# Kernel optimization log

Measured on AMD Instinct MI355X. Metric: run time of the kernel, lower is better.

The kernel has to match this reference:

```python
import jax, jax.numpy as jnp
from jax import lax
import numpy as np

V, E, NF = 50000, 300, 1          # vocab, embed_size, n_features
H = 256                            # hidden size (both layers)
B, TH, TB = 128, 32, 512           # batch, headline len, body len
NC = 4                             # n_classes


def setup_inputs() -> dict:
    key = jax.random.key(0)
    ks = jax.random.split(key, 24)
    emb = jax.random.normal(ks[0], (V, E), jnp.float32) * 0.1
    emb = emb.at[0].set(0.0)  # pad token -> zero row so seqlen masking is meaningful

    def make_ids(kid, klen, T):
        raw = jax.random.randint(kid, (B, T, NF), 1, V)
        lens = jax.random.randint(klen, (B,), max(T // 4, 1), T + 1)
        mask = jnp.arange(T)[None, :, None] < lens[:, None, None]
        return jnp.where(mask, raw, 0)

    headline_ids = make_ids(ks[1], ks[2], TH)
    body_ids = make_ids(ks[3], ks[4], TB)

    def gru_params(k, din, h):
        k1, k2 = jax.random.split(k, 2)
        s = 1.0 / np.sqrt(din + h)
        return (jax.random.normal(k1, (din + h, 2 * h), jnp.float32) * s,
                jnp.ones((2 * h,), jnp.float32),          # TF GRUCell gate bias init = 1.0
                jax.random.normal(k2, (din + h, h), jnp.float32) * s,
                jnp.zeros((h,), jnp.float32))

    D0 = NF * E
    hd0 = gru_params(ks[5], D0, H)
    hd1 = gru_params(ks[6], H, H)
    bd0 = gru_params(ks[7], D0, H)
    bd1 = gru_params(ks[8], H, H)

    W_pred = jax.random.normal(ks[9], (2 * H, NC), jnp.float32) * (1.0 / np.sqrt(2 * H))
    b_pred = jnp.zeros((NC,), jnp.float32)

    out = {"headline_ids": headline_ids, "body_ids": body_ids, "embeddings": emb,
           "W_pred": W_pred, "b_pred": b_pred}
    for pref, p in (("hd0", hd0), ("hd1", hd1), ("bd0", bd0), ("bd1", bd1)):
        out[pref + "_Wg"], out[pref + "_bg"], out[pref + "_Wc"], out[pref + "_bc"] = p
    return out


def _seq_length(x):
    # used = sign(max(|x|, axis=2)); seqlen = sum over time
    return jnp.sum(jnp.sign(jnp.max(jnp.abs(x), axis=2)), axis=1).astype(jnp.int32)


def _gru_layer(x, seqlen, Wg, bg, Wc, bc):
    # x: [B, T, D] -> outputs [B, T, H], final state [B, H]; dynamic_rnn semantics:
    # past seqlen, output is zero and state is copied through.
    Bsz, T, _ = x.shape
    Hh = Wc.shape[1]
    xt = jnp.swapaxes(x, 0, 1)  # [T, B, D]
    tids = jnp.arange(T)

    def step(h, inp):
        xi, t = inp
        xh = jnp.concatenate([xi, h], axis=-1)
        r, u = jnp.split(jax.nn.sigmoid(xh @ Wg + bg), 2, axis=-1)
        c = jnp.tanh(jnp.concatenate([xi, r * h], axis=-1) @ Wc + bc)
        nh = u * h + (1.0 - u) * c
        valid = (t < seqlen)[:, None]
        out = jnp.where(valid, nh, 0.0)
        h_next = jnp.where(valid, nh, h)
        return h_next, out

    h0 = jnp.zeros((Bsz, Hh), x.dtype)
    hf, outs = lax.scan(step, h0, (xt, tids))
    return jnp.swapaxes(outs, 0, 1), hf


def _stream(ids, emb, layers):
    x = emb[ids].reshape(ids.shape[0], ids.shape[1], -1)  # [B, T, NF*E]
    h = None
    for (Wg, bg, Wc, bc) in layers:
        sl = _seq_length(x)  # recomputed from current layer inputs, as in the source
        x, h = _gru_layer(x, sl, Wg, bg, Wc, bc)
    return h


def reference(headline_ids, body_ids, embeddings,
              hd0_Wg, hd0_bg, hd0_Wc, hd0_bc, hd1_Wg, hd1_bg, hd1_Wc, hd1_bc,
              bd0_Wg, bd0_bg, bd0_Wc, bd0_bc, bd1_Wg, bd1_bg, bd1_Wc, bd1_bc,
              W_pred, b_pred):
    h_head = _stream(headline_ids, embeddings,
                     [(hd0_Wg, hd0_bg, hd0_Wc, hd0_bc), (hd1_Wg, hd1_bg, hd1_Wc, hd1_bc)])
    h_body = _stream(body_ids, embeddings,
                     [(bd0_Wg, bd0_bg, bd0_Wc, bd0_bc), (bd1_Wg, bd1_bg, bd1_Wc, bd1_bc)])
    pred_input = jnp.concatenate([h_head, h_body], axis=1)  # [B, 2H]
    return pred_input @ W_pred + b_pred                      # [B, NC]
```

## Files before the change

kernel.cpp:

```cpp
#include <hip/hip_runtime.h>
#include <cstdint>
#include <cstddef>

#define H_    256
#define NG    768
#define BATCH 128
#define TH_   32
#define TB_   512
#define E_    300
#define RPB   16
#define NBLK  (BATCH / RPB)

typedef _Float16 half8 __attribute__((ext_vector_type(8)));
typedef float    floatx4 __attribute__((ext_vector_type(4)));

#define AS1 __attribute__((address_space(1)))
#define AS3 __attribute__((address_space(3)))

#define WC_LGKM0 0xC07F
#define WC_VM14  0x0F7E
#define WC_VM6   0x0F76
#define WC_VM0   0x0F70

__global__ __launch_bounds__(256) void pack_bias(
    const float* __restrict__ bg, const float* __restrict__ bc,
    float* __restrict__ bias)
{
  int idx = blockIdx.x * 256 + threadIdx.x;
  if (idx < NG) bias[idx] = (idx < 2 * H_) ? bg[idx] : bc[idx - 2 * H_];
}

__global__ __launch_bounds__(256) void pack_bx(
    const float* __restrict__ Wg, const float* __restrict__ Wc,
    int din, int KT, _Float16* __restrict__ out)
{
  int idx = blockIdx.x * 256 + threadIdx.x;
  if (idx >= KT * 48 * 64) return;
  int lane = idx & 63, tile = idx >> 6;
  int kt = tile / 48, nt = tile - kt * 48;
  int col = nt * 16 + (lane & 15);
  int k0 = kt * 32 + (lane >> 4) * 8;
  const float* W; int ncols, c2;
  if (col < 2 * H_) { W = Wg; ncols = 2 * H_; c2 = col; }
  else              { W = Wc; ncols = H_;     c2 = col - 2 * H_; }
  _Float16* dst = out + ((size_t)(kt * 48 + nt) * 64 + lane) * 8;
#pragma unroll
  for (int j = 0; j < 8; ++j) {
    int k = k0 + j;
    dst[j] = (k < din) ? (_Float16)W[(size_t)k * ncols + c2] : (_Float16)0.f;
  }
}

__global__ __launch_bounds__(256) void pack_w(
    const float* __restrict__ Wg, const float* __restrict__ Wc, int din,
    _Float16* __restrict__ wpk)
{
  int idx = blockIdx.x * 256 + threadIdx.x;
  if (idx >= 48 * 64) return;
  int tile = idx >> 6, lane = idx & 63;
  int grp = tile >> 4, tt = tile & 15;
  int wv = tt >> 1, s = tt & 1;
  const float* W; int ncols, n0;
  if (grp == 0)      { W = Wg; ncols = 2 * H_; n0 = wv * 32 + s * 16; }
  else if (grp == 1) { W = Wg; ncols = 2 * H_; n0 = 256 + wv * 32 + s * 16; }
  else               { W = Wc; ncols = H_;     n0 = wv * 32 + s * 16; }
  int n = n0 + (lane & 15);
  int kb = (lane >> 4) * 8;
#pragma unroll
  for (int kt = 0; kt < 8; ++kt) {
    _Float16* dst = wpk + ((size_t)(tile * 8 + kt) * 64 + lane) * 8;
#pragma unroll
    for (int j = 0; j < 8; ++j)
      dst[j] = (_Float16)W[(size_t)(din + kt * 32 + kb + j) * ncols + n];
  }
}

__global__ __launch_bounds__(256) void seq_k(const int* __restrict__ ids, int T,
                                             int* __restrict__ seq)
{
  __shared__ int red[256];
  int b = blockIdx.x, tid = threadIdx.x;
  int cnt = 0;
  for (int t = tid; t < T; t += 256) cnt += (ids[b * T + t] != 0) ? 1 : 0;
  red[tid] = cnt;
  __syncthreads();
  for (int s = 128; s > 0; s >>= 1) {
    if (tid < s) red[tid] += red[tid + s];
    __syncthreads();
  }
  if (tid == 0) seq[b] = red[0];
}

__global__ __launch_bounds__(256) void gemm_mfma(
    const float* __restrict__ Adir, const int* __restrict__ ids,
    const float* __restrict__ emb,
    const _Float16* __restrict__ Bpk, const float* __restrict__ bias,
    float* __restrict__ G, int K, int KT, int t0, int tcsh, int T)
{
  __shared__ __align__(16) _Float16 Al[2][64 * 40];
  __shared__ __align__(16) _Float16 Bl[2][8 * 512];
  const int tid = threadIdx.x;
  const int w = tid >> 6, lane = tid & 63;
  const int quad = lane >> 4, l15 = lane & 15;
  const int m0 = blockIdx.x * 64;
  const int n0 = blockIdx.y * 128;
  const int tc = 1 << tcsh;

  const int am = tid >> 2, akq = tid & 3;
  const int arow = m0 + am;
  const float* asrc;
  if (Adir) {
    asrc = Adir + (size_t)arow * K;
  } else {
    int b = arow >> tcsh, tl = arow & (tc - 1);
    asrc = emb + (size_t)ids[b * T + t0 + tl] * K;
  }

  float a8[8];
  auto loadA = [&](int kt) {
    int k0 = kt * 32 + akq * 8;
#pragma unroll
    for (int j = 0; j < 8; ++j) a8[j] = (k0 + j < K) ? asrc[k0 + j] : 0.f;
  };
  auto writeA = [&](int buf) {
    half8 v;
#pragma unroll
    for (int j = 0; j < 8; ++j) v[j] = (_Float16)a8[j];
    *(half8*)&Al[buf][am * 40 + akq * 8] = v;
  };
  auto stageB = [&](int kt, int buf) {
#pragma unroll
    for (int i = 0; i < 2; ++i) {
      int nt = (n0 >> 4) + w * 2 + i;
      const _Float16* src = Bpk + ((size_t)(kt * 48 + nt) * 64 + lane) * 8;
      __builtin_amdgcn_global_load_lds(
          (const AS1 unsigned int*)src,
          (AS3 unsigned int*)&Bl[buf][(w * 2 + i) * 512 + lane * 8], 16, 0, 0);
    }
  };

  loadA(0);
  stageB(0, 0);
  writeA(0);
  floatx4 acc[4][2] = {};

  for (int kt = 0; kt < KT; ++kt) {
    const int buf = kt & 1;
    __syncthreads();
    if (kt + 1 < KT) { loadA(kt + 1); stageB(kt + 1, buf ^ 1); }
    half8 bf0 = *(const half8*)&Bl[buf][(w * 2 + 0) * 512 + lane * 8];
    half8 bf1 = *(const half8*)&Bl[buf][(w * 2 + 1) * 512 + lane * 8];
#pragma unroll
    for (int st = 0; st < 4; ++st) {
      half8 af = *(const half8*)&Al[buf][(st * 16 + l15) * 40 + quad * 8];
      acc[st][0] = __builtin_amdgcn_mfma_f32_16x16x32_f16(af, bf0, acc[st][0], 0, 0, 0);
      acc[st][1] = __builtin_amdgcn_mfma_f32_16x16x32_f16(af, bf1, acc[st][1], 0, 0, 0);
    }
    if (kt + 1 < KT) writeA(buf ^ 1);
  }

  float bb[2] = { bias[n0 + w * 32 + l15], bias[n0 + w * 32 + 16 + l15] };
#pragma unroll
  for (int s = 0; s < 2; ++s) {
    int col = n0 + w * 32 + s * 16 + l15;
    int g = col >> 8, kk = col & 255;
    int ww = kk >> 5, ss = (kk >> 4) & 1, ll = kk & 15;
    int cc = 2 * g + ss;
#pragma unroll
    for (int st = 0; st < 4; ++st) {
#pragma unroll
      for (int r = 0; r < 4; ++r) {
        int grow = m0 + st * 16 + quad * 4 + r;
        int b = grow >> tcsh, tl = grow & (tc - 1);
        int rg = b >> 4, mm = b & 15, qb = mm >> 2, rb = mm & 3;
        G[((size_t)tl * BATCH + rg * RPB) * NG +
          ((ww * 6 + cc) * 64 + qb * 16 + ll) * 4 + rb] = acc[st][s][r] + bb[s];
      }
    }
  }
}

__global__ __launch_bounds__(512, 1) void gru_pers(
    const float* __restrict__ G0, const _Float16* __restrict__ W0,
    const int* __restrict__ q0, float* __restrict__ o0, float* __restrict__ s0,
    int t00, int tc0,
    const float* __restrict__ G1, const _Float16* __restrict__ W1,
    const int* __restrict__ q1, float* __restrict__ o1, float* __restrict__ s1,
    int t01, int tc1,
    const float* __restrict__ G2, const _Float16* __restrict__ W2,
    const int* __restrict__ q2, float* __restrict__ o2, float* __restrict__ s2,
    int t02, int tc2,
    const int* __restrict__ g_ids, const float* __restrict__ g_emb,
    const _Float16* __restrict__ g_Bpk, const float* __restrict__ g_bias,
    float* __restrict__ g_G, int g_KT, int g_t0, int g_tcsh, int g_T, int g_nbx)
{
  __shared__ __align__(16) char smem[114688];

  const int tid = threadIdx.x;

  if (blockIdx.x >= 3 * NBLK) {
    const int half = tid >> 8;
    _Float16* Al = (_Float16*)(smem + half * 10240);
    _Float16* Bl = (_Float16*)(smem + 20480 + half * 16384);
    const int t256 = tid & 255;
    const int w4 = (tid >> 6) & 3, lane = tid & 63;
    const int quad = lane >> 4, l15 = lane & 15;
    const int tidx = (blockIdx.x - 3 * NBLK) * 2 + half;
    const int bx = tidx % g_nbx, by = tidx / g_nbx;
    const int m0 = bx * 64, n0 = by * 128;
    const int tc = 1 << g_tcsh;

    const int am = t256 >> 2, akq = t256 & 3;
    const int arow = m0 + am;
    const int ab = arow >> g_tcsh, atl = arow & (tc - 1);
    const float* asrc = g_emb + (size_t)g_ids[ab * g_T + g_t0 + atl] * E_;

    float a8[8];
    auto loadA = [&](int kt) {
      int k0 = kt * 32 + akq * 8;
#pragma unroll
      for (int j = 0; j < 8; ++j) a8[j] = (k0 + j < E_) ? asrc[k0 + j] : 0.f;
    };
    auto writeA = [&](int buf) {
      half8 v;
#pragma unroll
      for (int j = 0; j < 8; ++j) v[j] = (_Float16)a8[j];
      *(half8*)&Al[buf * 2560 + am * 40 + akq * 8] = v;
    };
    auto stageB = [&](int kt, int buf) {
#pragma unroll
      for (int i = 0; i < 2; ++i) {
        int nt = (n0 >> 4) + w4 * 2 + i;
        const _Float16* src = g_Bpk + ((size_t)(kt * 48 + nt) * 64 + lane) * 8;
        __builtin_amdgcn_global_load_lds(
            (const AS1 unsigned int*)src,
            (AS3 unsigned int*)&Bl[buf * 4096 + (w4 * 2 + i) * 512 + lane * 8],
            16, 0, 0);
      }
    };

    loadA(0);
    stageB(0, 0);
    writeA(0);
    floatx4 acc[4][2] = {};

    for (int kt = 0; kt < g_KT; ++kt) {
      const int buf = kt & 1;
      __syncthreads();
      if (kt + 1 < g_KT) { loadA(kt + 1); stageB(kt + 1, buf ^ 1); }
      half8 bf0 = *(const half8*)&Bl[buf * 4096 + (w4 * 2 + 0) * 512 + lane * 8];
      half8 bf1 = *(const half8*)&Bl[buf * 4096 + (w4 * 2 + 1) * 512 + lane * 8];
#pragma unroll
      for (int st = 0; st < 4; ++st) {
        half8 af = *(const half8*)&Al[buf * 2560 + (st * 16 + l15) * 40 + quad * 8];
        acc[st][0] = __builtin_amdgcn_mfma_f32_16x16x32_f16(af, bf0, acc[st][0], 0, 0, 0);
        acc[st][1] = __builtin_amdgcn_mfma_f32_16x16x32_f16(af, bf1, acc[st][1], 0, 0, 0);
      }
      if (kt + 1 < g_KT) writeA(buf ^ 1);
    }

    float bb[2] = { g_bias[n0 + w4 * 32 + l15], g_bias[n0 + w4 * 32 + 16 + l15] };
#pragma unroll
    for (int s = 0; s < 2; ++s) {
      int col = n0 + w4 * 32 + s * 16 + l15;
      int g = col >> 8, kk = col & 255;
      int ww = kk >> 5, ss = (kk >> 4) & 1, ll = kk & 15;
      int cc = 2 * g + ss;
#pragma unroll
      for (int st = 0; st < 4; ++st) {
#pragma unroll
        for (int r = 0; r < 4; ++r) {
          int grow = m0 + st * 16 + quad * 4 + r;
          int b = grow >> g_tcsh, tl = grow & (tc - 1);
          int rg2 = b >> 4, mm = b & 15, qb = mm >> 2, rb = mm & 3;
          g_G[((size_t)tl * BATCH + rg2 * RPB) * NG +
              ((ww * 6 + cc) * 64 + qb * 16 + ll) * 4 + rb] = acc[st][s][r] + bb[s];
        }
      }
    }
    return;
  }

  _Float16* hpk = (_Float16*)smem;
  _Float16* rpk = (_Float16*)(smem + 8192);
  float* GsB = (float*)(smem + 16384);

  const int job = blockIdx.x >> 3, rg = blockIdx.x & 7;
  const float* G; const _Float16* Wsrc; const int* seq;
  float* outp; float* state; int t0, tcl;
  if (job == 0)      { G = G0; Wsrc = W0; seq = q0; outp = o0; state = s0; t0 = t00; tcl = tc0; }
  else if (job == 1) { G = G1; Wsrc = W1; seq = q1; outp = o1; state = s1; t0 = t01; tcl = tc1; }
  else               { G = G2; Wsrc = W2; seq = q2; outp = o2; state = s2; t0 = t02; tcl = tc2; }
  if (!G) return;

  const int w = tid >> 6, lane = tid & 63;
  const int quad = lane >> 4, l15 = lane & 15;

  floatx4 wg[4][8];
  floatx4 wc[2][8];
#pragma unroll
  for (int i = 0; i < 4; ++i) {
    const int tile = (i >> 1) * 16 + w * 2 + (i & 1);
#pragma unroll
    for (int kt = 0; kt < 8; ++kt) {
      wg[i][kt] = *(const floatx4*)&Wsrc[((size_t)(tile * 8 + kt) * 64 + lane) * 8];
      asm volatile("" : "+v"(wg[i][kt]));
    }
  }
#pragma unroll
  for (int i = 0; i < 2; ++i) {
    const int tile = 32 + w * 2 + i;
#pragma unroll
    for (int kt = 0; kt < 8; ++kt) {
      wc[i][kt] = *(const floatx4*)&Wsrc[((size_t)(tile * 8 + kt) * 64 + lane) * 8];
      asm volatile("" : "+a"(wc[i][kt]));
    }
  }

  int seq4[4];
#pragma unroll
  for (int r = 0; r < 4; ++r) seq4[r] = seq[rg * RPB + quad * 4 + r];
  int Smax = 0;
#pragma unroll
  for (int i = 0; i < 16; ++i) Smax = max(Smax, seq[rg * RPB + i]);
  int steps = Smax - t0;
  if (steps < 0) steps = 0;
  if (steps > tcl) steps = tcl;

  const int wbase = (w * 64 + quad * 2 + (l15 >> 3)) * 8 + (l15 & 7);
  const int rbase = (((quad >> 1) << 5) + ((l15 & 3) << 3) +
                     ((l15 >> 2) << 1) + (quad & 1)) * 8;

  float h_reg[2][4];
#pragma unroll
  for (int s = 0; s < 2; ++s)
#pragma unroll
    for (int r = 0; r < 4; ++r) {
      int row = quad * 4 + r, k = w * 32 + s * 16 + l15;
      float v = (t0 == 0) ? 0.f : state[(size_t)(rg * RPB + row) * H_ + k];
      h_reg[s][r] = v;
      hpk[wbase + s * 256 + r * 64] = (_Float16)v;
    }

  const float* gblk = G + (size_t)rg * RPB * NG + w * (6 * 256);
  float* ldsw = GsB + w * (6 * 256);
  auto stage = [&](int t, int buf) {
    const float* gp = gblk + (size_t)t * BATCH * NG;
    float* lp = ldsw + buf * 12288;
#pragma unroll
    for (int c = 0; c < 6; ++c) {
      __builtin_amdgcn_global_load_lds(
          (const AS1 unsigned int*)(gp + c * 256 + lane * 4),
          (AS3 unsigned int*)(lp + c * 256), 16, 0, 0);
    }
  };
  if (steps > 0) stage(0, 0);
  __syncthreads();

  const _Float16* hA = &hpk[rbase];
  const _Float16* rA = &rpk[rbase];

  for (int t = 0; t < steps; ++t) {
    const int buf = t & 1;
    const bool staged = (t + 1 < steps);
    if (staged) stage(t + 1, buf ^ 1);

    floatx4 acc[4] = {};
#pragma unroll
    for (int kt = 0; kt < 8; ++kt) {
      half8 a = *(const half8*)&hA[kt * 512];
#pragma unroll
      for (int s = 0; s < 4; ++s)
        acc[s] = __builtin_amdgcn_mfma_f32_16x16x32_f16(
            a, __builtin_bit_cast(half8, wg[s][kt]), acc[s], 0, 0, 0);
    }

    if (staged) {
      if (outp) __builtin_amdgcn_s_waitcnt(WC_VM14);
      else      __builtin_amdgcn_s_waitcnt(WC_VM6);
    } else {
      __builtin_amdgcn_s_waitcnt(WC_VM0);
    }

    floatx4 gA[4];
#pragma unroll
    for (int c = 0; c < 4; ++c)
      gA[c] = *(const floatx4*)&GsB[buf * 12288 + (w * 6 + c) * 256 + lane * 4];

#pragma unroll
    for (int s = 0; s < 2; ++s)
#pragma unroll
      for (int r = 0; r < 4; ++r) {
        float pre = acc[s][r] + gA[s][r];
        float g = __builtin_amdgcn_rcpf(1.f + __expf(-pre));
        rpk[wbase + s * 256 + r * 64] = (_Float16)(g * h_reg[s][r]);
      }
    float u_reg[2][4];
#pragma unroll
    for (int s = 0; s < 2; ++s)
#pragma unroll
      for (int r = 0; r < 4; ++r) {
        float pre = acc[2 + s][r] + gA[2 + s][r];
        u_reg[s][r] = __builtin_amdgcn_rcpf(1.f + __expf(-pre));
      }
    __builtin_amdgcn_s_waitcnt(WC_LGKM0);
    __builtin_amdgcn_s_barrier();

    floatx4 accB[2] = {};
#pragma unroll
    for (int kt = 0; kt < 8; ++kt) {
      half8 a = *(const half8*)&rA[kt * 512];
#pragma unroll
      for (int s = 0; s < 2; ++s)
        accB[s] = __builtin_amdgcn_mfma_f32_16x16x32_f16(
            a, __builtin_bit_cast(half8, wc[s][kt]), accB[s], 0, 0, 0);
    }
    floatx4 gB[2];
#pragma unroll
    for (int s = 0; s < 2; ++s)
      gB[s] = *(const floatx4*)&GsB[buf * 12288 + (w * 6 + 4 + s) * 256 + lane * 4];

#pragma unroll
    for (int s = 0; s < 2; ++s)
#pragma unroll
      for (int r = 0; r < 4; ++r) {
        int row = quad * 4 + r;
        float pre = accB[s][r] + gB[s][r];
        float c = 1.f - 2.f * __builtin_amdgcn_rcpf(1.f + __expf(2.f * pre));
        float u = u_reg[s][r];
        float hn = u * h_reg[s][r] + (1.f - u) * c;
        bool valid = (t0 + t) < seq4[r];
        hn = valid ? hn : h_reg[s][r];
        h_reg[s][r] = hn;
        hpk[wbase + s * 256 + r * 64] = (_Float16)hn;
        if (outp)
          outp[((size_t)(rg * RPB + row) * tcl + t) * H_ + (w * 32 + s * 16 + l15)] =
              valid ? hn : 0.f;
      }
    __builtin_amdgcn_s_waitcnt(WC_LGKM0);
    __builtin_amdgcn_s_barrier();
  }
#pragma unroll
  for (int s = 0; s < 2; ++s)
#pragma unroll
    for (int r = 0; r < 4; ++r)
      state[(size_t)(rg * RPB + quad * 4 + r) * H_ + (w * 32 + s * 16 + l15)] =
          h_reg[s][r];
}

__global__ __launch_bounds__(512) void pred_k(
    const float* __restrict__ hh, const float* __restrict__ hb,
    const float* __restrict__ Wp, const float* __restrict__ bpred,
    float* __restrict__ out)
{
  int tid = threadIdx.x;
  int b = tid >> 2, c = tid & 3;
  float acc = bpred[c];
  for (int k = 0; k < H_; ++k) acc += hh[b * H_ + k] * Wp[k * 4 + c];
  for (int k = 0; k < H_; ++k) acc += hb[b * H_ + k] * Wp[(H_ + k) * 4 + c];
  out[b * 4 + c] = acc;
}

extern "C" void kernel_launch(void* const* d_in, const int* in_sizes, int n_in,
                              void* d_out, int out_size, void* d_ws, size_t ws_size,
                              hipStream_t stream)
{
  (void)in_sizes; (void)n_in; (void)out_size;
  const int*   idsH = (const int*)  d_in[0];
  const int*   idsB = (const int*)  d_in[1];
  const float* emb  = (const float*)d_in[2];
  const float* Wp   = (const float*)d_in[3];
  const float* bp   = (const float*)d_in[4];
  const float* W[4][4];
  for (int s = 0; s < 4; ++s)
    for (int q = 0; q < 4; ++q)
      W[s][q] = (const float*)d_in[5 + s * 4 + q];

  auto rnd = [](size_t n) { return (n + 255) & ~(size_t)255; };
  auto need = [&](int ch, bool rider) -> size_t {
    size_t s = 0;
    s += rnd(BATCH) * 2;
    for (int i = 0; i < 4; ++i)
      s += rnd(NG) + rnd(98304) + rnd(122880);
    s += rnd((size_t)BATCH * H_) * 4;
    s += rnd((size_t)BATCH * ch * NG) * (rider ? 2 : 1);
    s += rnd((size_t)BATCH * ch * NG);
    s += rnd((size_t)BATCH * ch * H_);
    s += rnd((size_t)BATCH * TH_ * NG);
    s += rnd((size_t)BATCH * TH_ * H_);
    return s * 4;
  };

  int CH = 64;
  bool rider = need(64, true) <= ws_size;
  bool merged = rider || need(64, false) <= ws_size;
  if (!merged) {
    while (CH > 8 && need(CH, false) > ws_size) CH >>= 1;
    merged = (CH >= TH_);
  }
  const int CHH = (CH < TH_) ? CH : TH_;
  const int tcshB = __builtin_ctz(CH), tcshH = __builtin_ctz(CHH);

  float* wbase = (float*)d_ws;
  size_t off = 0;
  auto alloc = [&](size_t n) {
    float* p = wbase + off; off += rnd(n); return p;
  };
  int* seqH = (int*)alloc(BATCH);
  int* seqB = (int*)alloc(BATCH);
  float* bi[4]; _Float16* Wpk[4]; _Float16* Bxh[4];
  const int din[4] = {E_, H_, E_, H_};
  const int KT[4]  = {10, 8, 10, 8};
  for (int s = 0; s < 4; ++s) {
    bi[s]  = alloc(NG);
    Wpk[s] = (_Float16*)alloc(98304);
    Bxh[s] = (_Float16*)alloc(122880);
  }
  float* st0  = alloc((size_t)BATCH * H_);
  float* stH0 = alloc((size_t)BATCH * H_);
  float* hfH  = alloc((size_t)BATCH * H_);
  float* hfB  = alloc((size_t)BATCH * H_);
  float* Gc0b[2];
  Gc0b[0] = alloc((size_t)BATCH * CH * NG);
  Gc0b[1] = rider ? alloc((size_t)BATCH * CH * NG) : Gc0b[0];
  float* Gc1 = alloc((size_t)BATCH * CH * NG);
  float* Oc  = alloc((size_t)BATCH * CH * H_);
  float* GH1 = alloc((size_t)BATCH * TH_ * NG);
  float* OcH = alloc((size_t)BATCH * TH_ * H_);
  float* GH0 = Gc1;

  for (int s = 0; s < 4; ++s) {
    pack_bias<<<(NG + 255) / 256, 256, 0, stream>>>(W[s][1], W[s][3], bi[s]);
    pack_w<<<(48 * 64 + 255) / 256, 256, 0, stream>>>(
        W[s][0], W[s][2], din[s], Wpk[s]);
    pack_bx<<<(KT[s] * 48 * 64 + 255) / 256, 256, 0, stream>>>(
        W[s][0], W[s][2], din[s], KT[s], Bxh[s]);
  }
  seq_k<<<BATCH, 256, 0, stream>>>(idsH, TH_, seqH);
  seq_k<<<BATCH, 256, 0, stream>>>(idsB, TB_, seqB);

  const int nbx = BATCH * CH / 64;
  const int nrider = nbx * (NG / 128) / 2;

  auto gru3 = [&](const float* g0, const _Float16* w0, const int* x0, float* y0,
                  float* z0, int a0, int b0,
                  const float* g1, const _Float16* w1, const int* x1, float* y1,
                  float* z1, int a1, int b1,
                  const float* g2, const _Float16* w2, const int* x2, float* y2,
                  float* z2, int a2, int b2,
                  float* rG, int rt0) {
    int grid = 3 * NBLK + (rG ? nrider : 0);
    gru_pers<<<grid, 512, 0, stream>>>(g0, w0, x0, y0, z0, a0, b0,
                                       g1, w1, x1, y1, z1, a1, b1,
                                       g2, w2, x2, y2, z2, a2, b2,
                                       idsB, emb, Bxh[2], bi[2],
                                       rG, KT[2], rt0, tcshB, TB_, nbx);
  };

  if (merged) {
    dim3 ggH(BATCH * TH_ / 64, NG / 128);
    gemm_mfma<<<ggH, 256, 0, stream>>>(nullptr, idsH, emb, Bxh[0], bi[0],
                                       GH0, E_, KT[0], 0, 5, TH_);
    const int nch = TB_ / CH;
    dim3 gg(nbx, NG / 128);
    gemm_mfma<<<gg, 256, 0, stream>>>(nullptr, idsB, emb, Bxh[2], bi[2],
                                      Gc0b[0], E_, KT[2], 0, tcshB, TB_);
    for (int c = 0; c < nch; ++c) {
      int t0 = c * CH;
      if (!rider && c > 0)
        gemm_mfma<<<gg, 256, 0, stream>>>(nullptr, idsB, emb, Bxh[2], bi[2],
                                          Gc0b[0], E_, KT[2], t0, tcshB, TB_);
      const float* g2 = (c == 0) ? GH0 : (c == 1) ? GH1 : nullptr;
      bool ride = rider && (c + 1 < nch);
      gru3(Gc0b[rider ? (c & 1) : 0], Wpk[2], seqB, Oc, st0, t0, CH,
           (c > 0) ? Gc1 : nullptr, Wpk[3], seqB, nullptr, hfB, (c - 1) * CH, CH,
           g2, Wpk[(c == 0) ? 0 : 1], seqH,
           (c == 0) ? OcH : nullptr, (c == 0) ? stH0 : hfH, 0, TH_,
           ride ? Gc0b[(c + 1) & 1] : nullptr, (c + 1) * CH);
      if (c == 0)
        gemm_mfma<<<ggH, 256, 0, stream>>>(OcH, nullptr, nullptr, Bxh[1], bi[1],
                                           GH1, H_, KT[1], 0, 5, TH_);
      gemm_mfma<<<gg, 256, 0, stream>>>(Oc, nullptr, nullptr, Bxh[3], bi[3],
                                        Gc1, H_, KT[3], 0, tcshB, TB_);
    }
    gru3(nullptr, Wpk[2], seqB, nullptr, st0, 0, CH,
         Gc1, Wpk[3], seqB, nullptr, hfB, (nch - 1) * CH, CH,
         nullptr, Wpk[1], seqH, nullptr, hfH, 0, TH_,
         nullptr, 0);
  } else {
    auto run_stream = [&](const int* ids, int T, int chs, int tcsh,
                          const int* seq, int l0, int l1, float* hf) {
      int nchunks = T / chs;
      dim3 gg2(BATCH * chs / 64, NG / 128);
      for (int c = 0; c < nchunks; ++c) {
        int t0 = c * chs;
        gemm_mfma<<<gg2, 256, 0, stream>>>(nullptr, ids, emb, Bxh[l0], bi[l0],
                                           Gc0b[0], E_, KT[l0], t0, tcsh, T);
        gru3(Gc0b[0], Wpk[l0], seq, Oc, st0, t0, chs,
             (c > 0) ? Gc1 : nullptr, Wpk[l1], seq, nullptr, hf, (c - 1) * chs, chs,
             nullptr, Wpk[l1], seq, nullptr, hf, 0, chs,
             nullptr, 0);
        gemm_mfma<<<gg2, 256, 0, stream>>>(Oc, nullptr, nullptr, Bxh[l1], bi[l1],
                                           Gc1, H_, KT[l1], 0, tcsh, T);
      }
      gru3(nullptr, Wpk[l0], seq, nullptr, st0, 0, chs,
           Gc1, Wpk[l1], seq, nullptr, hf, (nchunks - 1) * chs, chs,
           nullptr, Wpk[l1], seq, nullptr, hf, 0, chs,
           nullptr, 0);
    };
    run_stream(idsH, TH_, CHH, tcshH, seqH, 0, 1, hfH);
    run_stream(idsB, TB_, CH,  tcshB, seqB, 2, 3, hfB);
  }

  pred_k<<<1, 512, 0, stream>>>(hfH, hfB, Wp, bp, (float*)d_out);
}
```

Measured before the change: 2.571 ms.

## Fold all chunk GEMMs into persistent GRU launches via three-job rider pipeline

Adds a full-pipeline mode with CH=32 and double-buffered layer-0 gates, layer-1 gates and layer-0 outputs. Each persistent GRU launch now also runs rider GEMM blocks: the next chunk's layer-0 input projection, the previous chunk's layer-1 input projection, and the headline layer-1 projection. This removes the standalone GEMM launches that serialised with the recurrence. The separate bias, weight-packing and seq-length kernels are merged into one pack_all launch. The cost is more workspace, more launches because chunks are smaller, and extra pipeline depth of two chunks.

Result: faster. 2.277 ms (median of 2 runs) (-11.4%).

```diff
diff --git a/kernel.cpp b/kernel.cpp
--- a/kernel.cpp
+++ b/kernel.cpp
@@ -22,41 +22,15 @@
 #define WC_VM6   0x0F76
 #define WC_VM0   0x0F70
 
-__global__ __launch_bounds__(256) void pack_bias(
-    const float* __restrict__ bg, const float* __restrict__ bc,
-    float* __restrict__ bias)
+__device__ __forceinline__ void d_bias(const float* bg, const float* bc,
+                                       float* bias, int idx)
 {
-  int idx = blockIdx.x * 256 + threadIdx.x;
-  if (idx < NG) bias[idx] = (idx < 2 * H_) ? bg[idx] : bc[idx - 2 * H_];
+  bias[idx] = (idx < 2 * H_) ? bg[idx] : bc[idx - 2 * H_];
 }
 
-__global__ __launch_bounds__(256) void pack_bx(
-    const float* __restrict__ Wg, const float* __restrict__ Wc,
-    int din, int KT, _Float16* __restrict__ out)
+__device__ __forceinline__ void d_packw(const float* Wg, const float* Wc,
+                                        int din, _Float16* wpk, int idx)
 {
-  int idx = blockIdx.x * 256 + threadIdx.x;
-  if (idx >= KT * 48 * 64) return;
-  int lane = idx & 63, tile = idx >> 6;
-  int kt = tile / 48, nt = tile - kt * 48;
-  int col = nt * 16 + (lane & 15);
-  int k0 = kt * 32 + (lane >> 4) * 8;
-  const float* W; int ncols, c2;
-  if (col < 2 * H_) { W = Wg; ncols = 2 * H_; c2 = col; }
-  else              { W = Wc; ncols = H_;     c2 = col - 2 * H_; }
-  _Float16* dst = out + ((size_t)(kt * 48 + nt) * 64 + lane) * 8;
-#pragma unroll
-  for (int j = 0; j < 8; ++j) {
-    int k = k0 + j;
-    dst[j] = (k < din) ? (_Float16)W[(size_t)k * ncols + c2] : (_Float16)0.f;
-  }
-}
-
-__global__ __launch_bounds__(256) void pack_w(
-    const float* __restrict__ Wg, const float* __restrict__ Wc, int din,
-    _Float16* __restrict__ wpk)
-{
-  int idx = blockIdx.x * 256 + threadIdx.x;
-  if (idx >= 48 * 64) return;
   int tile = idx >> 6, lane = idx & 63;
   int grp = tile >> 4, tt = tile & 15;
   int wv = tt >> 1, s = tt & 1;
@@ -75,20 +49,73 @@
   }
 }
 
-__global__ __launch_bounds__(256) void seq_k(const int* __restrict__ ids, int T,
-                                             int* __restrict__ seq)
+__device__ __forceinline__ void d_packbx(const float* Wg, const float* Wc,
+                                         int din, int KT, _Float16* out, int idx)
 {
-  __shared__ int red[256];
-  int b = blockIdx.x, tid = threadIdx.x;
-  int cnt = 0;
-  for (int t = tid; t < T; t += 256) cnt += (ids[b * T + t] != 0) ? 1 : 0;
-  red[tid] = cnt;
-  __syncthreads();
-  for (int s = 128; s > 0; s >>= 1) {
-    if (tid < s) red[tid] += red[tid + s];
+  int lane = idx & 63, tile = idx >> 6;
+  int kt = tile / 48, nt = tile - kt * 48;
+  int col = nt * 16 + (lane & 15);
+  int k0 = kt * 32 + (lane >> 4) * 8;
+  const float* W; int ncols, c2;
+  if (col < 2 * H_) { W = Wg; ncols = 2 * H_; c2 = col; }
+  else              { W = Wc; ncols = H_;     c2 = col - 2 * H_; }
+  _Float16* dst = out + ((size_t)(kt * 48 + nt) * 64 + lane) * 8;
+#pragma unroll
+  for (int j = 0; j < 8; ++j) {
+    int k = k0 + j;
+    dst[j] = (k < din) ? (_Float16)W[(size_t)k * ncols + c2] : (_Float16)0.f;
+  }
+}
+
+__global__ __launch_bounds__(256) void pack_all(
+    const int* __restrict__ idsH, const int* __restrict__ idsB,
+    int* __restrict__ seqH, int* __restrict__ seqB,
+    const float* Wg0, const float* bg0, const float* Wc0, const float* bc0,
+    const float* Wg1, const float* bg1, const float* Wc1, const float* bc1,
+    const float* Wg2, const float* bg2, const float* Wc2, const float* bc2,
+    const float* Wg3, const float* bg3, const float* Wc3, const float* bc3,
+    float* bi0, float* bi1, float* bi2, float* bi3,
+    _Float16* w0, _Float16* w1, _Float16* w2, _Float16* w3,
+    _Float16* x0, _Float16* x1, _Float16* x2, _Float16* x3)
+{
+  int blk = blockIdx.x, tid = threadIdx.x;
+  if (blk < 256) {
+    __shared__ int red[256];
+    const int* ids = (blk < 128) ? idsH : idsB;
+    int T = (blk < 128) ? TH_ : TB_;
+    int* seq = (blk < 128) ? seqH : seqB;
+    int b = blk & 127;
+    int cnt = 0;
+    for (int t = tid; t < T; t += 256) cnt += (ids[b * T + t] != 0) ? 1 : 0;
+    red[tid] = cnt;
     __syncthreads();
-  }
-  if (tid == 0) seq[b] = red[0];
+    for (int s = 128; s > 0; s >>= 1) {
+      if (tid < s) red[tid] += red[tid + s];
+      __syncthreads();
+    }
+    if (tid == 0) seq[b] = red[0];
+    return;
+  }
+  int idx = (blk - 256) * 256 + tid;
+  const float* Wg[4] = {Wg0, Wg1, Wg2, Wg3};
+  const float* bg[4] = {bg0, bg1, bg2, bg3};
+  const float* Wc[4] = {Wc0, Wc1, Wc2, Wc3};
+  const float* bc[4] = {bc0, bc1, bc2, bc3};
+  float* bi[4] = {bi0, bi1, bi2, bi3};
+  _Float16* wp[4] = {w0, w1, w2, w3};
+  _Float16* bx[4] = {x0, x1, x2, x3};
+  const int din[4] = {E_, H_, E_, H_};
+  const int KT[4] = {10, 8, 10, 8};
+#pragma unroll
+  for (int s = 0; s < 4; ++s) {
+    if (idx < NG) { d_bias(bg[s], bc[s], bi[s], idx); return; }
+    idx -= NG;
+    if (idx < 48 * 64) { d_packw(Wg[s], Wc[s], din[s], wp[s], idx); return; }
+    idx -= 48 * 64;
+    int szx = KT[s] * 48 * 64;
+    if (idx < szx) { d_packbx(Wg[s], Wc[s], din[s], KT[s], bx[s], idx); return; }
+    idx -= szx;
+  }
 }
 
 __global__ __launch_bounds__(256) void gemm_mfma(
@@ -190,36 +217,63 @@
     const float* __restrict__ G2, const _Float16* __restrict__ W2,
     const int* __restrict__ q2, float* __restrict__ o2, float* __restrict__ s2,
     int t02, int tc2,
-    const int* __restrict__ g_ids, const float* __restrict__ g_emb,
-    const _Float16* __restrict__ g_Bpk, const float* __restrict__ g_bias,
-    float* __restrict__ g_G, int g_KT, int g_t0, int g_tcsh, int g_T, int g_nbx)
+    const float* rA_A, const int* rA_ids, const _Float16* rA_B,
+    const float* rA_bi, float* rA_G, int rA_K, int rA_KT, int rA_t0,
+    int rA_nbx, int rA_nblk,
+    const float* rB_A, const int* rB_ids, const _Float16* rB_B,
+    const float* rB_bi, float* rB_G, int rB_K, int rB_KT, int rB_t0,
+    int rB_nbx, int rB_nblk,
+    const float* rC_A, const int* rC_ids, const _Float16* rC_B,
+    const float* rC_bi, float* rC_G, int rC_K, int rC_KT, int rC_t0,
+    int rC_nbx, int rC_nblk,
+    const float* __restrict__ r_emb, int r_tcsh, int r_T)
 {
   __shared__ __align__(16) char smem[114688];
 
   const int tid = threadIdx.x;
 
   if (blockIdx.x >= 3 * NBLK) {
+    int rb = blockIdx.x - 3 * NBLK;
+    const float* Adir; const int* ids; const _Float16* Bpk; const float* bias;
+    float* G; int K, KT, t0, nbx;
+    if (rb < rA_nblk) {
+      Adir = rA_A; ids = rA_ids; Bpk = rA_B; bias = rA_bi; G = rA_G;
+      K = rA_K; KT = rA_KT; t0 = rA_t0; nbx = rA_nbx;
+    } else if (rb < rA_nblk + rB_nblk) {
+      rb -= rA_nblk;
+      Adir = rB_A; ids = rB_ids; Bpk = rB_B; bias = rB_bi; G = rB_G;
+      K = rB_K; KT = rB_KT; t0 = rB_t0; nbx = rB_nbx;
+    } else {
+      rb -= rA_nblk + rB_nblk;
+      Adir = rC_A; ids = rC_ids; Bpk = rC_B; bias = rC_bi; G = rC_G;
+      K = rC_K; KT = rC_KT; t0 = rC_t0; nbx = rC_nbx;
+    }
     const int half = tid >> 8;
     _Float16* Al = (_Float16*)(smem + half * 10240);
     _Float16* Bl = (_Float16*)(smem + 20480 + half * 16384);
     const int t256 = tid & 255;
     const int w4 = (tid >> 6) & 3, lane = tid & 63;
     const int quad = lane >> 4, l15 = lane & 15;
-    const int tidx = (blockIdx.x - 3 * NBLK) * 2 + half;
-    const int bx = tidx % g_nbx, by = tidx / g_nbx;
+    const int tidx = rb * 2 + half;
+    const int bx = tidx % nbx, by = tidx / nbx;
     const int m0 = bx * 64, n0 = by * 128;
-    const int tc = 1 << g_tcsh;
+    const int tc = 1 << r_tcsh;
 
     const int am = t256 >> 2, akq = t256 & 3;
     const int arow = m0 + am;
-    const int ab = arow >> g_tcsh, atl = arow & (tc - 1);
-    const float* asrc = g_emb + (size_t)g_ids[ab * g_T + g_t0 + atl] * E_;
+    const float* asrc;
+    if (Adir) {
+      asrc = Adir + (size_t)arow * K;
+    } else {
+      int ab = arow >> r_tcsh, atl = arow & (tc - 1);
+      asrc = r_emb + (size_t)ids[ab * r_T + t0 + atl] * K;
+    }
 
     float a8[8];
     auto loadA = [&](int kt) {
       int k0 = kt * 32 + akq * 8;
 #pragma unroll
-      for (int j = 0; j < 8; ++j) a8[j] = (k0 + j < E_) ? asrc[k0 + j] : 0.f;
+      for (int j = 0; j < 8; ++j) a8[j] = (k0 + j < K) ? asrc[k0 + j] : 0.f;
     };
     auto writeA = [&](int buf) {
       half8 v;
@@ -231,7 +285,7 @@
 #pragma unroll
       for (int i = 0; i < 2; ++i) {
         int nt = (n0 >> 4) + w4 * 2 + i;
-        const _Float16* src = g_Bpk + ((size_t)(kt * 48 + nt) * 64 + lane) * 8;
+        const _Float16* src = Bpk + ((size_t)(kt * 48 + nt) * 64 + lane) * 8;
         __builtin_amdgcn_global_load_lds(
             (const AS1 unsigned int*)src,
             (AS3 unsigned int*)&Bl[buf * 4096 + (w4 * 2 + i) * 512 + lane * 8],
@@ -244,10 +298,10 @@
     writeA(0);
     floatx4 acc[4][2] = {};
 
-    for (int kt = 0; kt < g_KT; ++kt) {
+    for (int kt = 0; kt < KT; ++kt) {
       const int buf = kt & 1;
       __syncthreads();
-      if (kt + 1 < g_KT) { loadA(kt + 1); stageB(kt + 1, buf ^ 1); }
+      if (kt + 1 < KT) { loadA(kt + 1); stageB(kt + 1, buf ^ 1); }
       half8 bf0 = *(const half8*)&Bl[buf * 4096 + (w4 * 2 + 0) * 512 + lane * 8];
       half8 bf1 = *(const half8*)&Bl[buf * 4096 + (w4 * 2 + 1) * 512 + lane * 8];
 #pragma unroll
@@ -256,10 +310,10 @@
         acc[st][0] = __builtin_amdgcn_mfma_f32_16x16x32_f16(af, bf0, acc[st][0], 0, 0, 0);
         acc[st][1] = __builtin_amdgcn_mfma_f32_16x16x32_f16(af, bf1, acc[st][1], 0, 0, 0);
       }
-      if (kt + 1 < g_KT) writeA(buf ^ 1);
-    }
-
-    float bb[2] = { g_bias[n0 + w4 * 32 + l15], g_bias[n0 + w4 * 32 + 16 + l15] };
+      if (kt + 1 < KT) writeA(buf ^ 1);
+    }
+
+    float bb[2] = { bias[n0 + w4 * 32 + l15], bias[n0 + w4 * 32 + 16 + l15] };
 #pragma unroll
     for (int s = 0; s < 2; ++s) {
       int col = n0 + w4 * 32 + s * 16 + l15;
@@ -271,10 +325,10 @@
 #pragma unroll
         for (int r = 0; r < 4; ++r) {
           int grow = m0 + st * 16 + quad * 4 + r;
-          int b = grow >> g_tcsh, tl = grow & (tc - 1);
-          int rg2 = b >> 4, mm = b & 15, qb = mm >> 2, rb = mm & 3;
-          g_G[((size_t)tl * BATCH + rg2 * RPB) * NG +
-              ((ww * 6 + cc) * 64 + qb * 16 + ll) * 4 + rb] = acc[st][s][r] + bb[s];
+          int b = grow >> r_tcsh, tl = grow & (tc - 1);
+          int rg2 = b >> 4, mm = b & 15, qb = mm >> 2, rb2 = mm & 3;
+          G[((size_t)tl * BATCH + rg2 * RPB) * NG +
+            ((ww * 6 + cc) * 64 + qb * 16 + ll) * 4 + rb2] = acc[st][s][r] + bb[s];
         }
       }
     }
@@ -477,12 +531,20 @@
       W[s][q] = (const float*)d_in[5 + s * 4 + q];
 
   auto rnd = [](size_t n) { return (n + 255) & ~(size_t)255; };
-  auto need = [&](int ch, bool rider) -> size_t {
-    size_t s = 0;
-    s += rnd(BATCH) * 2;
-    for (int i = 0; i < 4; ++i)
-      s += rnd(NG) + rnd(98304) + rnd(122880);
-    s += rnd((size_t)BATCH * H_) * 4;
+  const size_t prefix_f =
+      2 * rnd(BATCH) + 4 * (rnd(NG) + rnd(98304) + rnd(122880)) +
+      4 * rnd((size_t)BATCH * H_);
+  auto need_full = [&]() -> size_t {
+    size_t s = prefix_f;
+    s += 2 * rnd((size_t)BATCH * 32 * NG);
+    s += 2 * rnd((size_t)BATCH * 32 * NG);
+    s += 2 * rnd((size_t)BATCH * 32 * H_);
+    s += 2 * rnd((size_t)BATCH * TH_ * NG);
+    s += rnd((size_t)BATCH * TH_ * H_);
+    return s * 4;
+  };
+  auto need_r2 = [&](int ch, bool rider) -> size_t {
+    size_t s = prefix_f;
     s += rnd((size_t)BATCH * ch * NG) * (rider ? 2 : 1);
     s += rnd((size_t)BATCH * ch * NG);
     s += rnd((size_t)BATCH * ch * H_);
@@ -491,12 +553,14 @@
     return s * 4;
   };
 
-  int CH = 64;
-  bool rider = need(64, true) <= ws_size;
-  bool merged = rider || need(64, false) <= ws_size;
-  if (!merged) {
-    while (CH > 8 && need(CH, false) > ws_size) CH >>= 1;
-    merged = (CH >= TH_);
+  enum { M_FULL, M_R2, M_SERIAL } mode;
+  int CH = 64; bool rider = false;
+  if (need_full() <= ws_size) { mode = M_FULL; CH = 32; }
+  else if (need_r2(64, true) <= ws_size) { mode = M_R2; CH = 64; rider = true; }
+  else {
+    CH = 64;
+    while (CH > 8 && need_r2(CH, false) > ws_size) CH >>= 1;
+    mode = (CH >= TH_) ? M_R2 : M_SERIAL;
   }
   const int CHH = (CH < TH_) ? CH : TH_;
   const int tcshB = __builtin_ctz(CH), tcshH = __builtin_ctz(CHH);
@@ -509,7 +573,6 @@
   int* seqH = (int*)alloc(BATCH);
   int* seqB = (int*)alloc(BATCH);
   float* bi[4]; _Float16* Wpk[4]; _Float16* Bxh[4];
-  const int din[4] = {E_, H_, E_, H_};
   const int KT[4]  = {10, 8, 10, 8};
   for (int s = 0; s < 4; ++s) {
     bi[s]  = alloc(NG);
@@ -520,49 +583,105 @@
   float* stH0 = alloc((size_t)BATCH * H_);
   float* hfH  = alloc((size_t)BATCH * H_);
   float* hfB  = alloc((size_t)BATCH * H_);
-  float* Gc0b[2];
-  Gc0b[0] = alloc((size_t)BATCH * CH * NG);
-  Gc0b[1] = rider ? alloc((size_t)BATCH * CH * NG) : Gc0b[0];
-  float* Gc1 = alloc((size_t)BATCH * CH * NG);
-  float* Oc  = alloc((size_t)BATCH * CH * H_);
-  float* GH1 = alloc((size_t)BATCH * TH_ * NG);
-  float* OcH = alloc((size_t)BATCH * TH_ * H_);
-  float* GH0 = Gc1;
-
-  for (int s = 0; s < 4; ++s) {
-    pack_bias<<<(NG + 255) / 256, 256, 0, stream>>>(W[s][1], W[s][3], bi[s]);
-    pack_w<<<(48 * 64 + 255) / 256, 256, 0, stream>>>(
-        W[s][0], W[s][2], din[s], Wpk[s]);
-    pack_bx<<<(KT[s] * 48 * 64 + 255) / 256, 256, 0, stream>>>(
-        W[s][0], W[s][2], din[s], KT[s], Bxh[s]);
-  }
-  seq_k<<<BATCH, 256, 0, stream>>>(idsH, TH_, seqH);
-  seq_k<<<BATCH, 256, 0, stream>>>(idsB, TB_, seqB);
-
-  const int nbx = BATCH * CH / 64;
-  const int nrider = nbx * (NG / 128) / 2;
-
-  auto gru3 = [&](const float* g0, const _Float16* w0, const int* x0, float* y0,
-                  float* z0, int a0, int b0,
-                  const float* g1, const _Float16* w1, const int* x1, float* y1,
-                  float* z1, int a1, int b1,
-                  const float* g2, const _Float16* w2, const int* x2, float* y2,
-                  float* z2, int a2, int b2,
-                  float* rG, int rt0) {
-    int grid = 3 * NBLK + (rG ? nrider : 0);
-    gru_pers<<<grid, 512, 0, stream>>>(g0, w0, x0, y0, z0, a0, b0,
-                                       g1, w1, x1, y1, z1, a1, b1,
-                                       g2, w2, x2, y2, z2, a2, b2,
-                                       idsB, emb, Bxh[2], bi[2],
-                                       rG, KT[2], rt0, tcshB, TB_, nbx);
-  };
-
-  if (merged) {
+
+  float *Gc0b[2], *Gc1b[2], *Ocb[2], *GH0, *GH1, *OcH;
+  if (mode == M_FULL) {
+    Gc0b[0] = alloc((size_t)BATCH * CH * NG);
+    Gc0b[1] = alloc((size_t)BATCH * CH * NG);
+    Gc1b[0] = alloc((size_t)BATCH * CH * NG);
+    Gc1b[1] = alloc((size_t)BATCH * CH * NG);
+    Ocb[0]  = alloc((size_t)BATCH * CH * H_);
+    Ocb[1]  = alloc((size_t)BATCH * CH * H_);
+    GH0     = alloc((size_t)BATCH * TH_ * NG);
+    GH1     = alloc((size_t)BATCH * TH_ * NG);
+    OcH     = alloc((size_t)BATCH * TH_ * H_);
+  } else {
+    Gc0b[0] = alloc((size_t)BATCH * CH * NG);
+    Gc0b[1] = rider ? alloc((size_t)BATCH * CH * NG) : Gc0b[0];
+    Gc1b[0] = Gc1b[1] = alloc((size_t)BATCH * CH * NG);
+    Ocb[0]  = Ocb[1]  = alloc((size_t)BATCH * CH * H_);
+    GH1     = alloc((size_t)BATCH * TH_ * NG);
+    OcH     = alloc((size_t)BATCH * TH_ * H_);
+    GH0     = Gc1b[0];
+  }
+
+  {
+    int packN = 0;
+    for (int s = 0; s < 4; ++s) packN += NG + 48 * 64 + KT[s] * 48 * 64;
+    int grid = 256 + (packN + 255) / 256;
+    pack_all<<<grid, 256, 0, stream>>>(
+        idsH, idsB, seqH, seqB,
+        W[0][0], W[0][1], W[0][2], W[0][3],
+        W[1][0], W[1][1], W[1][2], W[1][3],
+        W[2][0], W[2][1], W[2][2], W[2][3],
+        W[3][0], W[3][1], W[3][2], W[3][3],
+        bi[0], bi[1], bi[2], bi[3],
+        Wpk[0], Wpk[1], Wpk[2], Wpk[3],
+        Bxh[0], Bxh[1], Bxh[2], Bxh[3]);
+  }
+
+  struct RJ {
+    const float* A; const int* ids; const _Float16* B; const float* bi;
+    float* G; int K, KT, t0, nbx, nblk;
+  };
+  auto gru_launch = [&](const float* g0, const _Float16* w0, const int* x0,
+                        float* y0, float* z0, int a0, int b0,
+                        const float* g1, const _Float16* w1, const int* x1,
+                        float* y1, float* z1, int a1, int b1,
+                        const float* g2, const _Float16* w2, const int* x2,
+                        float* y2, float* z2, int a2, int b2,
+                        RJ rA, RJ rB, RJ rC, int tcsh) {
+    int grid = 3 * NBLK + rA.nblk + rB.nblk + rC.nblk;
+    gru_pers<<<grid, 512, 0, stream>>>(
+        g0, w0, x0, y0, z0, a0, b0,
+        g1, w1, x1, y1, z1, a1, b1,
+        g2, w2, x2, y2, z2, a2, b2,
+        rA.A, rA.ids, rA.B, rA.bi, rA.G, rA.K, rA.KT, rA.t0, rA.nbx, rA.nblk,
+        rB.A, rB.ids, rB.B, rB.bi, rB.G, rB.K, rB.KT, rB.t0, rB.nbx, rB.nblk,
+        rC.A, rC.ids, rC.B, rC.bi, rC.G, rC.K, rC.KT, rC.t0, rC.nbx, rC.nblk,
+        emb, tcsh, TB_);
+  };
+  const RJ RNULL = {nullptr, nullptr, nullptr, nullptr, nullptr, 0, 0, 0, 1, 0};
+
+  if (mode == M_FULL) {
+    const int nch = TB_ / CH;
+    const int nbx = BATCH * CH / 64;
+    const int nrb = nbx * (NG / 128) / 2;
+    gemm_mfma<<<dim3(nbx, NG / 128), 256, 0, stream>>>(
+        nullptr, idsB, emb, Bxh[2], bi[2], Gc0b[0], E_, KT[2], 0, tcshB, TB_);
+    gemm_mfma<<<dim3(BATCH * TH_ / 64, NG / 128), 256, 0, stream>>>(
+        nullptr, idsH, emb, Bxh[0], bi[0], GH0, E_, KT[0], 0, tcshH, TH_);
+
+    for (int c = 0; c <= nch + 1; ++c) {
+      const float* g0 = (c < nch) ? Gc0b[c & 1] : nullptr;
+      const float* g1 = (c >= 2) ? Gc1b[c & 1] : nullptr;
+      const float* g2 = (c == 0) ? GH0 : (c == 2) ? GH1 : nullptr;
+      RJ rA = RNULL, rB = RNULL, rC = RNULL;
+      if (c + 1 < nch)
+        rA = {nullptr, idsB, Bxh[2], bi[2], Gc0b[(c + 1) & 1],
+              E_, KT[2], (c + 1) * CH, nbx, nrb};
+      if (c >= 1 && c <= nch)
+        rB = {Ocb[(c - 1) & 1], nullptr, Bxh[3], bi[3], Gc1b[(c - 1) & 1],
+              H_, KT[3], 0, nbx, nrb};
+      if (c == 1)
+        rC = {OcH, nullptr, Bxh[1], bi[1], GH1, H_, KT[1], 0,
+              BATCH * TH_ / 64, (BATCH * TH_ / 64) * (NG / 128) / 2};
+
+      gru_launch(
+          g0, Wpk[2], seqB, (c < nch) ? Ocb[c & 1] : nullptr, st0, c * CH, CH,
+          g1, Wpk[3], seqB, nullptr, hfB, (c - 2) * CH, CH,
+          g2, Wpk[(c == 0) ? 0 : 1], seqH,
+          (c == 0) ? OcH : nullptr, (c == 0) ? stH0 : hfH, 0, TH_,
+          rA, rB, rC, tcshB);
+    }
+  } else if (mode == M_R2) {
+    const int nch = TB_ / CH;
+    const int nbx = BATCH * CH / 64;
+    const int nrb = rider ? nbx * (NG / 128) / 2 : 0;
     dim3 ggH(BATCH * TH_ / 64, NG / 128);
+    dim3 gg(nbx, NG / 128);
     gemm_mfma<<<ggH, 256, 0, stream>>>(nullptr, idsH, emb, Bxh[0], bi[0],
-                                       GH0, E_, KT[0], 0, 5, TH_);
-    const int nch = TB_ / CH;
-    dim3 gg(nbx, NG / 128);
+                                       GH0, E_, KT[0], 0, tcshH, TH_);
     gemm_mfma<<<gg, 256, 0, stream>>>(nullptr, idsB, emb, Bxh[2], bi[2],
                                       Gc0b[0], E_, KT[2], 0, tcshB, TB_);
     for (int c = 0; c < nch; ++c) {
@@ -571,22 +690,27 @@
         gemm_mfma<<<gg, 256, 0, stream>>>(nullptr, idsB, emb, Bxh[2], bi[2],
                                           Gc0b[0], E_, KT[2], t0, tcshB, TB_);
       const float* g2 = (c == 0) ? GH0 : (c == 1) ? GH1 : nullptr;
-      bool ride = rider && (c + 1 < nch);
-      gru3(Gc0b[rider ? (c & 1) : 0], Wpk[2], seqB, Oc, st0, t0, CH,
-           (c > 0) ? Gc1 : nullptr, Wpk[3], seqB, nullptr, hfB, (c - 1) * CH, CH,
-           g2, Wpk[(c == 0) ? 0 : 1], seqH,
-           (c == 0) ? OcH : nullptr, (c == 0) ? stH0 : hfH, 0, TH_,
-           ride ? Gc0b[(c + 1) & 1] : nullptr, (c + 1) * CH);
+      RJ rA = RNULL;
+      if (rider && c + 1 < nch)
+        rA = {nullptr, idsB, Bxh[2], bi[2], Gc0b[(c + 1) & 1],
+              E_, KT[2], (c + 1) * CH, nbx, nrb};
+      gru_launch(
+          Gc0b[rider ? (c & 1) : 0], Wpk[2], seqB, Ocb[0], st0, t0, CH,
+          (c > 0) ? Gc1b[0] : nullptr, Wpk[3], seqB, nullptr, hfB,
+          (c - 1) * CH, CH,
+          g2, Wpk[(c == 0) ? 0 : 1], seqH,
+          (c == 0) ? OcH : nullptr, (c == 0) ? stH0 : hfH, 0, TH_,
+          rA, RNULL, RNULL, tcshB);
       if (c == 0)
         gemm_mfma<<<ggH, 256, 0, stream>>>(OcH, nullptr, nullptr, Bxh[1], bi[1],
-                                           GH1, H_, KT[1], 0, 5, TH_);
-      gemm_mfma<<<gg, 256, 0, stream>>>(Oc, nullptr, nullptr, Bxh[3], bi[3],
-                                        Gc1, H_, KT[3], 0, tcshB, TB_);
-    }
-    gru3(nullptr, Wpk[2], seqB, nullptr, st0, 0, CH,
-         Gc1, Wpk[3], seqB, nullptr, hfB, (nch - 1) * CH, CH,
-         nullptr, Wpk[1], seqH, nullptr, hfH, 0, TH_,
-         nullptr, 0);
+                                           GH1, H_, KT[1], 0, tcshH, TH_);
+      gemm_mfma<<<gg, 256, 0, stream>>>(Ocb[0], nullptr, nullptr, Bxh[3], bi[3],
+                                        Gc1b[0], H_, KT[3], 0, tcshB, TB_);
+    }
+    gru_launch(nullptr, Wpk[2], seqB, nullptr, st0, 0, CH,
+               Gc1b[0], Wpk[3], seqB, nullptr, hfB, (nch - 1) * CH, CH,
+               nullptr, Wpk[1], seqH, nullptr, hfH, 0, TH_,
+               RNULL, RNULL, RNULL, tcshB);
   } else {
     auto run_stream = [&](const int* ids, int T, int chs, int tcsh,
                           const int* seq, int l0, int l1, float* hf) {
@@ -596,17 +720,18 @@
         int t0 = c * chs;
         gemm_mfma<<<gg2, 256, 0, stream>>>(nullptr, ids, emb, Bxh[l0], bi[l0],
                                            Gc0b[0], E_, KT[l0], t0, tcsh, T);
-        gru3(Gc0b[0], Wpk[l0], seq, Oc, st0, t0, chs,
-             (c > 0) ? Gc1 : nullptr, Wpk[l1], seq, nullptr, hf, (c - 1) * chs, chs,
-             nullptr, Wpk[l1], seq, nullptr, hf, 0, chs,
-             nullptr, 0);
-        gemm_mfma<<<gg2, 256, 0, stream>>>(Oc, nullptr, nullptr, Bxh[l1], bi[l1],
-                                           Gc1, H_, KT[l1], 0, tcsh, T);
+        gru_launch(Gc0b[0], Wpk[l0], seq, Ocb[0], st0, t0, chs,
+                   (c > 0) ? Gc1b[0] : nullptr, Wpk[l1], seq, nullptr, hf,
+                   (c - 1) * chs, chs,
+                   nullptr, Wpk[l1], seq, nullptr, hf, 0, chs,
+                   RNULL, RNULL, RNULL, tcsh);
+        gemm_mfma<<<gg2, 256, 0, stream>>>(Ocb[0], nullptr, nullptr, Bxh[l1],
+                                           bi[l1], Gc1b[0], H_, KT[l1], 0, tcsh, T);
       }
-      gru3(nullptr, Wpk[l0], seq, nullptr, st0, 0, chs,
-           Gc1, Wpk[l1], seq, nullptr, hf, (nchunks - 1) * chs, chs,
-           nullptr, Wpk[l1], seq, nullptr, hf, 0, chs,
-           nullptr, 0);
+      gru_launch(nullptr, Wpk[l0], seq, nullptr, st0, 0, chs,
+                 Gc1b[0], Wpk[l1], seq, nullptr, hf, (nchunks - 1) * chs, chs,
+                 nullptr, Wpk[l1], seq, nullptr, hf, 0, chs,
+                 RNULL, RNULL, RNULL, tcsh);
     };
     run_stream(idsH, TH_, CHH, tcshH, seqH, 0, 1, hfH);
     run_stream(idsB, TB_, CH,  tcshB, seqB, 2, 3, hfB);
```
